# Kernel optimization log

Measured on AMD Instinct MI355X. Metric: run time of the kernel, lower is better.

## Reference

```python
import jax, jax.numpy as jnp
import numpy as np

B, T, D = 8, 4096, 768
H, HD, K = 12, 64, 32
TAU, THRESH = 12.5, 0.5
A_PARAM, B_PARAM, DT = 0.7, 0.8, 1.0  # nn.Parameters read via .item() -> scalar constants
N_FHN_STEPS = 2


def setup_inputs() -> dict:
    key = jax.random.key(0)
    k0, k1, k2, k3 = jax.random.split(key, 4)
    x = jax.random.normal(k0, (B, T, D), jnp.float32)
    spectral_basis = jax.random.normal(k1, (B, T, K), jnp.float32)
    w_qkv = jax.random.normal(k2, (3 * D, D), jnp.float32) * 0.02
    w_out = jax.random.normal(k3, (D, D), jnp.float32) * 0.02
    spectral_filter = jnp.ones((H, 32), jnp.float32) * 0.5
    return {"x": x, "spectral_basis": spectral_basis, "w_qkv": w_qkv,
            "w_out": w_out, "spectral_filter": spectral_filter}


def _fhn(stim):
    # Original expands stim [b,h,k] -> [b,h,k,head_dim] (constant along d), runs FHN,
    # then means over d. Values are identical along d, so amax over d == |stim| and the
    # mean is the identity; the math collapses exactly to per-element dynamics on [b,h,k].
    scale = jnp.maximum(jnp.abs(stim), 1e-6)          # == abs().amax(-1).clamp(1e-6)
    stim_normed = stim / scale
    gate = jax.nn.sigmoid((jnp.abs(stim) - THRESH) * 10.0)
    I = stim_normed * (0.1 + 0.9 * gate)
    alpha = DT / TAU
    denom = 1.0 + alpha * B_PARAM
    v = jnp.zeros_like(stim)
    w = jnp.zeros_like(stim)
    for _ in range(N_FHN_STEPS):  # fixed small n_steps, unrolled
        dv = v - (v * v * v) / 3.0 - w + I
        v_next = v + dv * DT
        w_next = (w + (v_next + A_PARAM) * alpha) / denom
        v = jnp.clip(v_next, -3.0, 3.0)
        w = jnp.clip(w_next, -3.0, 3.0)
    return v * scale


def reference(x, spectral_basis, w_qkv, w_out, spectral_filter):
    Bs, Ts, Ds = x.shape
    k = spectral_basis.shape[-1]
    qkv = x @ w_qkv.T                                   # [B,T,3D]
    qkv = qkv.reshape(Bs, Ts, 3, H, HD).transpose(2, 0, 3, 1, 4)  # three,b,h,t,d
    q, kk, v = qkv[0], qkv[1], qkv[2]
    q_spec = jnp.einsum('bhtd,btk->bhkd', q, spectral_basis)
    k_spec = jnp.einsum('bhtd,btk->bhkd', kk, spectral_basis)
    attn_spec = jnp.einsum('bhkd,bhkd->bhk', q_spec, k_spec) / (HD ** 0.5)
    filt = jax.nn.sigmoid(spectral_filter[:, :k])       # [H,k]
    attn_spec = attn_spec * filt[None, :, :]
    fhn_response = _fhn(attn_spec)                      # [B,H,k]
    v_spec = jnp.einsum('bhtd,btk->bhkd', v, spectral_basis)
    out_spec = fhn_response[..., None] * v_spec         # [B,H,k,d]
    out = jnp.einsum('bhkd,btk->bhtd', out_spec, spectral_basis)
    out = out.transpose(0, 2, 1, 3).reshape(Bs, Ts, Ds)  # b t (h d)
    return out @ w_out.T
```

## Files before the change

### kernel.cpp

```cpp
#include <hip/hip_runtime.h>

#define Bc 8
#define Tc 4096
#define Dc 768
#define Hc 12
#define HDc 64
#define Kc 32
#define TD3 2304
#define WQKV_F (TD3 * Dc)
#define WALL_F ((TD3 + Dc) * Dc)
#define XS_F (Bc * Kc * Dc)

typedef __attribute__((ext_vector_type(8))) short short8;
typedef __attribute__((ext_vector_type(4))) short short4v;
typedef __attribute__((ext_vector_type(4))) float float4v;

__device__ __forceinline__ float bf2f(unsigned short u) {
    unsigned v = ((unsigned)u) << 16;
    return __builtin_bit_cast(float, v);
}
__device__ __forceinline__ unsigned short f2bf(float f) {
    unsigned u = __builtin_bit_cast(unsigned, f);
    u += 0x7FFFu + ((u >> 16) & 1u);
    return (unsigned short)(u >> 16);
}
__device__ __forceinline__ void split8(const float* p, short8& hi, short8& lo) {
#pragma unroll
    for (int i = 0; i < 8; ++i) {
        unsigned short h = f2bf(p[i]);
        hi[i] = (short)h;
        lo[i] = (short)f2bf(p[i] - bf2f(h));
    }
}
__device__ __forceinline__ void split4(const float4v v, short4v& h, short4v& l) {
#pragma unroll
    for (int q = 0; q < 4; ++q) {
        unsigned short hb = f2bf(v[q]);
        h[q] = (short)hb;
        l[q] = (short)f2bf(v[q] - bf2f(hb));
    }
}

__global__ __launch_bounds__(256) void k1_fused(const float* __restrict__ x,
                                                const float* __restrict__ sb,
                                                const float* __restrict__ wqkv,
                                                const float* __restrict__ wout,
                                                float* __restrict__ pb,
                                                short* __restrict__ w_hi,
                                                short* __restrict__ w_lo) {
    __shared__ float xt[32 * 193];
    __shared__ float st[32 * 33];

    int tid = threadIdx.x;
    int bid = blockIdx.x;

    if (bid >= 512) {
        int i = ((bid - 512) * 256 + tid) * 4;
        const float* src = (i < WQKV_F) ? (wqkv + i) : (wout + (i - WQKV_F));
        float4v v = *(const float4v*)src;
        short4v h, l;
        split4(v, h, l);
        *(short4v*)(w_hi + i) = h;
        *(short4v*)(w_lo + i) = l;
        return;
    }

    int w    = tid >> 6;
    int lane = tid & 63;
    int col  = lane & 15;
    int quad = lane >> 4;

    int b  = bid >> 6;
    int dt = (bid >> 4) & 3;
    int tc = bid & 15;
    int d0 = dt * 192;
    size_t bT = (size_t)b * Tc + (size_t)tc * 256;

    float4v acc[2][3];
#pragma unroll
    for (int mi = 0; mi < 2; ++mi)
#pragma unroll
        for (int ni = 0; ni < 3; ++ni) acc[mi][ni] = (float4v){0.f, 0.f, 0.f, 0.f};

    for (int ks = 0; ks < 8; ++ks) {
        __syncthreads();
#pragma unroll
        for (int i = 0; i < 6; ++i) {
            int f4  = tid + i * 256;
            int row = f4 / 48, c4 = f4 % 48;
            float4v v = *(const float4v*)&x[(bT + ks * 32 + row) * Dc + d0 + c4 * 4];
#pragma unroll
            for (int q = 0; q < 4; ++q) xt[row * 193 + c4 * 4 + q] = v[q];
        }
        {
            int row = tid >> 3, c4 = tid & 7;
            float4v v = *(const float4v*)&sb[(bT + ks * 32 + row) * Kc + c4 * 4];
#pragma unroll
            for (int q = 0; q < 4; ++q) st[row * 33 + c4 * 4 + q] = v[q];
        }
        __syncthreads();

        short8 ah[2], al[2];
#pragma unroll
        for (int mi = 0; mi < 2; ++mi) {
            float av[8];
#pragma unroll
            for (int j = 0; j < 8; ++j)
                av[j] = st[(quad * 8 + j) * 33 + mi * 16 + col];
            split8(av, ah[mi], al[mi]);
        }
#pragma unroll
        for (int ni = 0; ni < 3; ++ni) {
            int nc = (w * 3 + ni) * 16 + col;
            float bv[8];
#pragma unroll
            for (int j = 0; j < 8; ++j)
                bv[j] = xt[(quad * 8 + j) * 193 + nc];
            short8 bh, bl;
            split8(bv, bh, bl);
#pragma unroll
            for (int mi = 0; mi < 2; ++mi) {
                acc[mi][ni] = __builtin_amdgcn_mfma_f32_16x16x32_bf16(ah[mi], bh, acc[mi][ni], 0, 0, 0);
                acc[mi][ni] = __builtin_amdgcn_mfma_f32_16x16x32_bf16(al[mi], bh, acc[mi][ni], 0, 0, 0);
                acc[mi][ni] = __builtin_amdgcn_mfma_f32_16x16x32_bf16(ah[mi], bl, acc[mi][ni], 0, 0, 0);
            }
        }
    }

    float* pbp = pb + (size_t)tc * XS_F;
#pragma unroll
    for (int mi = 0; mi < 2; ++mi)
#pragma unroll
        for (int ni = 0; ni < 3; ++ni)
#pragma unroll
            for (int r = 0; r < 4; ++r) {
                int kk = mi * 16 + quad * 4 + r;
                int dd = d0 + (w * 3 + ni) * 16 + col;
                pbp[((size_t)(b * Kc + kk)) * Dc + dd] = acc[mi][ni][r];
            }
}

__global__ __launch_bounds__(256) void k1r_reduce(const float* __restrict__ pb,
                                                  short* __restrict__ xs_hi,
                                                  short* __restrict__ xs_lo) {
    int i = (blockIdx.x * 256 + threadIdx.x) * 4;
    float4v s = (float4v){0.f, 0.f, 0.f, 0.f};
#pragma unroll
    for (int p = 0; p < 16; ++p) {
        float4v v = *(const float4v*)(pb + (size_t)p * XS_F + i);
#pragma unroll
        for (int q = 0; q < 4; ++q) s[q] += v[q];
    }
    short4v h, l;
    split4(s, h, l);
    *(short4v*)(xs_hi + i) = h;
    *(short4v*)(xs_lo + i) = l;
}

__global__ __launch_bounds__(256) void k2_qkv(const short* __restrict__ xs_hi,
                                              const short* __restrict__ xs_lo,
                                              const short* __restrict__ w_hi,
                                              const short* __restrict__ w_lo,
                                              float* __restrict__ c1) {
    int lane = threadIdx.x & 63;
    int w    = threadIdx.x >> 6;
    int m    = lane & 15, quad = lane >> 4;
    int mb = blockIdx.x & 7;
    int nb = blockIdx.x >> 3;
    int m0 = mb * 32;
    int n0 = nb * 64 + w * 16;

    const short* a0h = xs_hi + (size_t)(m0 + m) * Dc + quad * 8;
    const short* a0l = xs_lo + (size_t)(m0 + m) * Dc + quad * 8;
    const short* a1h = a0h + (size_t)16 * Dc;
    const short* a1l = a0l + (size_t)16 * Dc;
    const short* bhp = w_hi + (size_t)(n0 + m) * Dc + quad * 8;
    const short* blp = w_lo + (size_t)(n0 + m) * Dc + quad * 8;

    float4v acc0 = (float4v){0.f, 0.f, 0.f, 0.f};
    float4v acc1 = (float4v){0.f, 0.f, 0.f, 0.f};
#pragma unroll 4
    for (int s = 0; s < 24; ++s) {
        short8 bh = *(const short8*)(bhp + s * 32);
        short8 bl = *(const short8*)(blp + s * 32);
        short8 h0 = *(const short8*)(a0h + s * 32);
        short8 l0 = *(const short8*)(a0l + s * 32);
        short8 h1 = *(const short8*)(a1h + s * 32);
        short8 l1 = *(const short8*)(a1l + s * 32);
        acc0 = __builtin_amdgcn_mfma_f32_16x16x32_bf16(h0, bh, acc0, 0, 0, 0);
        acc0 = __builtin_amdgcn_mfma_f32_16x16x32_bf16(l0, bh, acc0, 0, 0, 0);
        acc0 = __builtin_amdgcn_mfma_f32_16x16x32_bf16(h0, bl, acc0, 0, 0, 0);
        acc1 = __builtin_amdgcn_mfma_f32_16x16x32_bf16(h1, bh, acc1, 0, 0, 0);
        acc1 = __builtin_amdgcn_mfma_f32_16x16x32_bf16(l1, bh, acc1, 0, 0, 0);
        acc1 = __builtin_amdgcn_mfma_f32_16x16x32_bf16(h1, bl, acc1, 0, 0, 0);
    }
    float* cp0 = c1 + (size_t)(m0 + quad * 4) * TD3 + n0 + m;
    float* cp1 = cp0 + (size_t)16 * TD3;
#pragma unroll
    for (int r = 0; r < 4; ++r) {
        cp0[(size_t)r * TD3] = acc0[r];
        cp1[(size_t)r * TD3] = acc1[r];
    }
}

__global__ __launch_bounds__(256) void k3_fhn(const float* __restrict__ c1,
                                              const float* __restrict__ sfilt,
                                              float* __restrict__ fhn) {
    int idx = blockIdx.x * 256 + threadIdx.x;
    if (idx >= Bc * Hc * Kc) return;
    int kk = idx & 31;
    int bh = idx >> 5;
    int h  = bh % Hc;
    int r  = (bh / Hc) * Kc + kk;

    const float* qp = c1 + (size_t)r * TD3 + h * HDc;
    const float* kp = qp + Dc;
    float s = 0.f;
#pragma unroll
    for (int dd = 0; dd < HDc; ++dd) s = fmaf(qp[dd], kp[dd], s);
    s *= 0.125f;

    float filt = 1.f / (1.f + __expf(-sfilt[h * 32 + kk]));
    s *= filt;

    float as    = fabsf(s);
    float scale = fmaxf(as, 1e-6f);
    float sn    = s / scale;
    float gate  = 1.f / (1.f + __expf(-(as - 0.5f) * 10.f));
    float I     = sn * (0.1f + 0.9f * gate);
    const float alpha = 0.08f;
    const float denom = 1.064f;
    float v = 0.f, w = 0.f;
#pragma unroll
    for (int it = 0; it < 2; ++it) {
        float dv = v - (v * v * v) / 3.f - w + I;
        float vn = v + dv;
        float wn = (w + (vn + 0.7f) * alpha) / denom;
        v = fminf(fmaxf(vn, -3.f), 3.f);
        w = fminf(fmaxf(wn, -3.f), 3.f);
    }
    fhn[idx] = v * scale;
}

__global__ __launch_bounds__(256) void k4_proj(const float* __restrict__ c1,
                                               const float* __restrict__ fhn,
                                               const short* __restrict__ wo_hi,
                                               const short* __restrict__ wo_lo,
                                               float* __restrict__ proj) {
    int wave = blockIdx.x * 4 + (threadIdx.x >> 6);
    int lane = threadIdx.x & 63;
    int mb = wave & 15;
    int nt = wave >> 4;
    int m0 = mb * 16, n0 = nt * 16;
    int m = lane & 15, quad = lane >> 4;

    const short* bhp = wo_hi + (size_t)(n0 + m) * Dc + quad * 8;
    const short* blp = wo_lo + (size_t)(n0 + m) * Dc + quad * 8;

    int r = m0 + m;
    int b = r >> 5, kk = r & 31;
    const float* apx = c1 + (size_t)r * TD3 + 2 * Dc + quad * 8;
    const float* fp  = fhn + (size_t)b * Hc * Kc + kk;

    float4v acc = (float4v){0.f, 0.f, 0.f, 0.f};
#pragma unroll 4
    for (int s = 0; s < 24; ++s) {
        int h = (s * 32 + quad * 8) >> 6;
        float f = fp[h * Kc];
        float av[8];
#pragma unroll
        for (int i = 0; i < 8; ++i) av[i] = apx[s * 32 + i] * f;
        short8 ah, al;
        split8(av, ah, al);
        short8 bh = *(const short8*)(bhp + s * 32);
        short8 bl = *(const short8*)(blp + s * 32);
        acc = __builtin_amdgcn_mfma_f32_16x16x32_bf16(ah, bh, acc, 0, 0, 0);
        acc = __builtin_amdgcn_mfma_f32_16x16x32_bf16(al, bh, acc, 0, 0, 0);
        acc = __builtin_amdgcn_mfma_f32_16x16x32_bf16(ah, bl, acc, 0, 0, 0);
    }
    float* cp = proj + (size_t)(m0 + quad * 4) * Dc + n0 + m;
#pragma unroll
    for (int rr = 0; rr < 4; ++rr) cp[(size_t)rr * Dc] = acc[rr];
}

__global__ __launch_bounds__(256) void k5_out(const float* __restrict__ proj,
                                              const float* __restrict__ sb,
                                              float* __restrict__ out) {
    __shared__ float pt[32 * 193];

    int tid  = threadIdx.x;
    int w    = tid >> 6;
    int lane = tid & 63;
    int col  = lane & 15;
    int quad = lane >> 4;

    int bid = blockIdx.x;
    int b  = bid >> 8;
    int tt = (bid >> 2) & 63;
    int et = bid & 3;
    int t0 = tt * 64 + w * 16;
    int e0 = et * 192;

#pragma unroll
    for (int i = 0; i < 6; ++i) {
        int f4  = tid + i * 256;
        int row = f4 / 48, c4 = f4 % 48;
        float4v v = *(const float4v*)&proj[(size_t)b * Kc * Dc + (size_t)row * Dc + e0 + c4 * 4];
#pragma unroll
        for (int q = 0; q < 4; ++q) pt[row * 193 + c4 * 4 + q] = v[q];
    }

    const float* apx = sb + ((size_t)b * Tc + t0 + col) * Kc + quad * 8;
    short8 ah, al;
    split8(apx, ah, al);

    __syncthreads();

    float4v acc[12];
#pragma unroll
    for (int ni = 0; ni < 12; ++ni) acc[ni] = (float4v){0.f, 0.f, 0.f, 0.f};

#pragma unroll
    for (int ni = 0; ni < 12; ++ni) {
        float bv[8];
#pragma unroll
        for (int j = 0; j < 8; ++j)
            bv[j] = pt[(quad * 8 + j) * 193 + ni * 16 + col];
        short8 bh, bl;
        split8(bv, bh, bl);
        acc[ni] = __builtin_amdgcn_mfma_f32_16x16x32_bf16(ah, bh, acc[ni], 0, 0, 0);
        acc[ni] = __builtin_amdgcn_mfma_f32_16x16x32_bf16(al, bh, acc[ni], 0, 0, 0);
        acc[ni] = __builtin_amdgcn_mfma_f32_16x16x32_bf16(ah, bl, acc[ni], 0, 0, 0);
    }

    float* op = out + ((size_t)b * Tc + t0 + quad * 4) * Dc + e0 + col;
#pragma unroll
    for (int ni = 0; ni < 12; ++ni)
#pragma unroll
        for (int r = 0; r < 4; ++r)
            op[(size_t)r * Dc + ni * 16] = acc[ni][r];
}

extern "C" void kernel_launch(void* const* d_in, const int* in_sizes, int n_in,
                              void* d_out, int out_size, void* d_ws, size_t ws_size,
                              hipStream_t stream) {
    const float* x     = (const float*)d_in[0];
    const float* sb    = (const float*)d_in[1];
    const float* wqkv  = (const float*)d_in[2];
    const float* wout  = (const float*)d_in[3];
    const float* sfilt = (const float*)d_in[4];
    float* out = (float*)d_out;

    float* pb    = (float*)d_ws;
    short* w_hi  = (short*)(pb + (size_t)16 * XS_F);
    short* w_lo  = w_hi + (size_t)WALL_F;
    short* xs_hi = w_lo + (size_t)WALL_F;
    short* xs_lo = xs_hi + (size_t)XS_F;
    float* c1    = (float*)(xs_lo + (size_t)XS_F);
    float* fhn   = c1 + (size_t)Bc * Kc * TD3;
    float* proj  = fhn + (size_t)Bc * Hc * Kc;

    const short* wo_hi = w_hi + (size_t)WQKV_F;
    const short* wo_lo = w_lo + (size_t)WQKV_F;

    hipLaunchKernelGGL(k1_fused,   dim3(2816), dim3(256), 0, stream,
                       x, sb, wqkv, wout, pb, w_hi, w_lo);
    hipLaunchKernelGGL(k1r_reduce, dim3(192),  dim3(256), 0, stream, pb, xs_hi, xs_lo);
    hipLaunchKernelGGL(k2_qkv,     dim3(288),  dim3(256), 0, stream, xs_hi, xs_lo, w_hi, w_lo, c1);
    hipLaunchKernelGGL(k3_fhn,     dim3(12),   dim3(256), 0, stream, c1, sfilt, fhn);
    hipLaunchKernelGGL(k4_proj,    dim3(192),  dim3(256), 0, stream, c1, fhn, wo_hi, wo_lo, proj);
    hipLaunchKernelGGL(k5_out,     dim3(2048), dim3(256), 0, stream, proj, sb, out);
}
```

Measured before the change: 259.0 us.

## Fuse FHN into projection kernel and emit transposed bf16 split projection

```diff
diff --git a/kernel.cpp b/kernel.cpp
--- a/kernel.cpp
+++ b/kernel.cpp
@@ -203,70 +203,72 @@
     }
 }
 
-__global__ __launch_bounds__(256) void k3_fhn(const float* __restrict__ c1,
-                                              const float* __restrict__ sfilt,
-                                              float* __restrict__ fhn) {
-    int idx = blockIdx.x * 256 + threadIdx.x;
-    if (idx >= Bc * Hc * Kc) return;
-    int kk = idx & 31;
-    int bh = idx >> 5;
-    int h  = bh % Hc;
-    int r  = (bh / Hc) * Kc + kk;
-
-    const float* qp = c1 + (size_t)r * TD3 + h * HDc;
-    const float* kp = qp + Dc;
-    float s = 0.f;
-#pragma unroll
-    for (int dd = 0; dd < HDc; ++dd) s = fmaf(qp[dd], kp[dd], s);
-    s *= 0.125f;
-
-    float filt = 1.f / (1.f + __expf(-sfilt[h * 32 + kk]));
-    s *= filt;
-
-    float as    = fabsf(s);
-    float scale = fmaxf(as, 1e-6f);
-    float sn    = s / scale;
-    float gate  = 1.f / (1.f + __expf(-(as - 0.5f) * 10.f));
-    float I     = sn * (0.1f + 0.9f * gate);
-    const float alpha = 0.08f;
-    const float denom = 1.064f;
-    float v = 0.f, w = 0.f;
-#pragma unroll
-    for (int it = 0; it < 2; ++it) {
-        float dv = v - (v * v * v) / 3.f - w + I;
-        float vn = v + dv;
-        float wn = (w + (vn + 0.7f) * alpha) / denom;
-        v = fminf(fmaxf(vn, -3.f), 3.f);
-        w = fminf(fmaxf(wn, -3.f), 3.f);
-    }
-    fhn[idx] = v * scale;
-}
-
 __global__ __launch_bounds__(256) void k4_proj(const float* __restrict__ c1,
-                                               const float* __restrict__ fhn,
+                                               const float* __restrict__ sfilt,
                                                const short* __restrict__ wo_hi,
                                                const short* __restrict__ wo_lo,
-                                               float* __restrict__ proj) {
-    int wave = blockIdx.x * 4 + (threadIdx.x >> 6);
-    int lane = threadIdx.x & 63;
+                                               short* __restrict__ pT_hi,
+                                               short* __restrict__ pT_lo) {
+    __shared__ float fh[64][13];
+    int tid = threadIdx.x;
+    int r0  = 64 * (blockIdx.x & 3);
+
+    for (int u = tid; u < 768; u += 256) {
+        int h = u >> 6, row_l = u & 63;
+        int r = r0 + row_l;
+        int kk = r & 31;
+        const float* qp = c1 + (size_t)r * TD3 + h * HDc;
+        const float* kp = qp + Dc;
+        float s = 0.f;
+#pragma unroll
+        for (int dd = 0; dd < HDc; dd += 4) {
+            float4v qv = *(const float4v*)(qp + dd);
+            float4v kv = *(const float4v*)(kp + dd);
+#pragma unroll
+            for (int q2 = 0; q2 < 4; ++q2) s = fmaf(qv[q2], kv[q2], s);
+        }
+        s *= 0.125f;
+        float filt = 1.f / (1.f + __expf(-sfilt[h * 32 + kk]));
+        s *= filt;
+        float as    = fabsf(s);
+        float scale = fmaxf(as, 1e-6f);
+        float sn    = s / scale;
+        float gate  = 1.f / (1.f + __expf(-(as - 0.5f) * 10.f));
+        float I     = sn * (0.1f + 0.9f * gate);
+        const float alpha = 0.08f;
+        const float denom = 1.064f;
+        float v = 0.f, w = 0.f;
+#pragma unroll
+        for (int it = 0; it < 2; ++it) {
+            float dv = v - (v * v * v) / 3.f - w + I;
+            float vn = v + dv;
+            float wn = (w + (vn + 0.7f) * alpha) / denom;
+            v = fminf(fmaxf(vn, -3.f), 3.f);
+            w = fminf(fmaxf(wn, -3.f), 3.f);
+        }
+        fh[row_l][h] = v * scale;
+    }
+    __syncthreads();
+
+    int wave = blockIdx.x * 4 + (tid >> 6);
+    int lane = tid & 63;
     int mb = wave & 15;
     int nt = wave >> 4;
     int m0 = mb * 16, n0 = nt * 16;
     int m = lane & 15, quad = lane >> 4;
+    int row_l = (tid >> 6) * 16 + m;
 
     const short* bhp = wo_hi + (size_t)(n0 + m) * Dc + quad * 8;
     const short* blp = wo_lo + (size_t)(n0 + m) * Dc + quad * 8;
 
     int r = m0 + m;
-    int b = r >> 5, kk = r & 31;
     const float* apx = c1 + (size_t)r * TD3 + 2 * Dc + quad * 8;
-    const float* fp  = fhn + (size_t)b * Hc * Kc + kk;
 
     float4v acc = (float4v){0.f, 0.f, 0.f, 0.f};
 #pragma unroll 4
     for (int s = 0; s < 24; ++s) {
         int h = (s * 32 + quad * 8) >> 6;
-        float f = fp[h * Kc];
+        float f = fh[row_l][h];
         float av[8];
 #pragma unroll
         for (int i = 0; i < 8; ++i) av[i] = apx[s * 32 + i] * f;
@@ -278,16 +280,17 @@
         acc = __builtin_amdgcn_mfma_f32_16x16x32_bf16(al, bh, acc, 0, 0, 0);
         acc = __builtin_amdgcn_mfma_f32_16x16x32_bf16(ah, bl, acc, 0, 0, 0);
     }
-    float* cp = proj + (size_t)(m0 + quad * 4) * Dc + n0 + m;
-#pragma unroll
-    for (int rr = 0; rr < 4; ++rr) cp[(size_t)rr * Dc] = acc[rr];
-}
-
-__global__ __launch_bounds__(256) void k5_out(const float* __restrict__ proj,
+    short4v hv, lv;
+    split4(acc, hv, lv);
+    size_t o = (size_t)(n0 + m) * (Bc * Kc) + m0 + quad * 4;
+    *(short4v*)(pT_hi + o) = hv;
+    *(short4v*)(pT_lo + o) = lv;
+}
+
+__global__ __launch_bounds__(256) void k5_out(const short* __restrict__ pT_hi,
+                                              const short* __restrict__ pT_lo,
                                               const float* __restrict__ sb,
                                               float* __restrict__ out) {
-    __shared__ float pt[32 * 193];
-
     int tid  = threadIdx.x;
     int w    = tid >> 6;
     int lane = tid & 63;
@@ -301,33 +304,19 @@
     int t0 = tt * 64 + w * 16;
     int e0 = et * 192;
 
-#pragma unroll
-    for (int i = 0; i < 6; ++i) {
-        int f4  = tid + i * 256;
-        int row = f4 / 48, c4 = f4 % 48;
-        float4v v = *(const float4v*)&proj[(size_t)b * Kc * Dc + (size_t)row * Dc + e0 + c4 * 4];
-#pragma unroll
-        for (int q = 0; q < 4; ++q) pt[row * 193 + c4 * 4 + q] = v[q];
-    }
-
     const float* apx = sb + ((size_t)b * Tc + t0 + col) * Kc + quad * 8;
     short8 ah, al;
     split8(apx, ah, al);
 
-    __syncthreads();
-
     float4v acc[12];
 #pragma unroll
     for (int ni = 0; ni < 12; ++ni) acc[ni] = (float4v){0.f, 0.f, 0.f, 0.f};
 
 #pragma unroll
     for (int ni = 0; ni < 12; ++ni) {
-        float bv[8];
-#pragma unroll
-        for (int j = 0; j < 8; ++j)
-            bv[j] = pt[(quad * 8 + j) * 193 + ni * 16 + col];
-        short8 bh, bl;
-        split8(bv, bh, bl);
+        size_t bo = (size_t)(e0 + ni * 16 + col) * (Bc * Kc) + b * 32 + quad * 8;
+        short8 bh = *(const short8*)(pT_hi + bo);
+        short8 bl = *(const short8*)(pT_lo + bo);
         acc[ni] = __builtin_amdgcn_mfma_f32_16x16x32_bf16(ah, bh, acc[ni], 0, 0, 0);
         acc[ni] = __builtin_amdgcn_mfma_f32_16x16x32_bf16(al, bh, acc[ni], 0, 0, 0);
         acc[ni] = __builtin_amdgcn_mfma_f32_16x16x32_bf16(ah, bl, acc[ni], 0, 0, 0);
@@ -357,8 +346,8 @@
     short* xs_hi = w_lo + (size_t)WALL_F;
     short* xs_lo = xs_hi + (size_t)XS_F;
     float* c1    = (float*)(xs_lo + (size_t)XS_F);
-    float* fhn   = c1 + (size_t)Bc * Kc * TD3;
-    float* proj  = fhn + (size_t)Bc * Hc * Kc;
+    short* pT_hi = (short*)(c1 + (size_t)Bc * Kc * TD3);
+    short* pT_lo = pT_hi + (size_t)XS_F;
 
     const short* wo_hi = w_hi + (size_t)WQKV_F;
     const short* wo_lo = w_lo + (size_t)WQKV_F;
@@ -367,7 +356,6 @@
                        x, sb, wqkv, wout, pb, w_hi, w_lo);
     hipLaunchKernelGGL(k1r_reduce, dim3(192),  dim3(256), 0, stream, pb, xs_hi, xs_lo);
     hipLaunchKernelGGL(k2_qkv,     dim3(288),  dim3(256), 0, stream, xs_hi, xs_lo, w_hi, w_lo, c1);
-    hipLaunchKernelGGL(k3_fhn,     dim3(12),   dim3(256), 0, stream, c1, sfilt, fhn);
-    hipLaunchKernelGGL(k4_proj,    dim3(192),  dim3(256), 0, stream, c1, fhn, wo_hi, wo_lo, proj);
-    hipLaunchKernelGGL(k5_out,     dim3(2048), dim3(256), 0, stream, proj, sb, out);
-}
+    hipLaunchKernelGGL(k4_proj,    dim3(192),  dim3(256), 0, stream, c1, sfilt, wo_hi, wo_lo, pT_hi, pT_lo);
+    hipLaunchKernelGGL(k5_out,     dim3(2048), dim3(256), 0, stream, pT_hi, pT_lo, sb, out);
+}
```

Measured after the change: 282.2 us. +9.0%, slower.
